# Performance work log

Hardware: AMD Instinct MI355X
Metric: run time of the kernel (lower is better)

The kernel has to match this reference:

```python
import jax, jax.numpy as jnp
import numpy as np

N = 100000
D = 128
R = 4
E = 1600000
LN_EPS = 1e-3  # keras LayerNormalization default epsilon


def setup_inputs() -> dict:
    key = jax.random.key(0)
    ks = jax.random.split(key, 12)
    return {
        "node_embeddings": jax.random.normal(ks[0], (N, D), jnp.float32),
        "rel_embeddings": jax.random.normal(ks[1], (R, D), jnp.float32),
        "adj_rows": jax.random.randint(ks[2], (R, E), 0, N, jnp.int32),
        "adj_cols": jax.random.randint(ks[3], (R, E), 0, N, jnp.int32),
        "adj_vals": jax.random.uniform(ks[4], (R, E), jnp.float32),
        "W_fuse": jax.random.normal(ks[5], (2 * D, D), jnp.float32) * 0.05,
        "b_fuse": jnp.zeros((D,), jnp.float32),
        "W_rel": jax.random.normal(ks[6], (R, D, D), jnp.float32) * 0.05,
        "b_rel": jnp.zeros((R, D), jnp.float32),
        "rel_weights": jnp.ones((R,), jnp.float32),
        "W_gate": jax.random.normal(ks[7], (D, D), jnp.float32) * 0.05,
        "b_gate": jnp.zeros((D,), jnp.float32),
        "ln_gamma": jnp.ones((D,), jnp.float32),
        "ln_beta": jnp.zeros((D,), jnp.float32),
    }


def reference(node_embeddings, rel_embeddings, adj_rows, adj_cols, adj_vals,
              W_fuse, b_fuse, W_rel, b_rel, rel_weights, W_gate, b_gate,
              ln_gamma, ln_beta):
    n = node_embeddings.shape[0]
    rel_outs = []
    for r in range(R):  # small fixed relation count, structurally distinct kernels
        # sparse-dense matmul: messages[i] = sum_j A_r[i,j] * X[j]
        gathered = adj_vals[r][:, None] * node_embeddings[adj_cols[r]]  # [E, D]
        messages = jax.ops.segment_sum(gathered, adj_rows[r], num_segments=n)  # [N, D]
        rel_vec = jnp.broadcast_to(rel_embeddings[r], messages.shape)
        cat = jnp.concatenate([messages, rel_vec], axis=-1)  # [N, 2D]
        fused = jax.nn.relu(cat @ W_fuse + b_fuse)  # [N, D]
        rel_outs.append(fused @ W_rel[r] + b_rel[r])  # relation-specific kernel
    stacked = jnp.stack(rel_outs, axis=0)  # [R, N, D]
    w = jax.nn.softmax(rel_weights)
    combined = jnp.einsum('r,rnd->nd', w, stacked)
    gate = jax.nn.sigmoid(node_embeddings @ W_gate + b_gate)
    x = node_embeddings + gate * combined
    mu = jnp.mean(x, axis=-1, keepdims=True)
    var = jnp.mean((x - mu) ** 2, axis=-1, keepdims=True)
    out = (x - mu) * jax.lax.rsqrt(var + LN_EPS) * ln_gamma + ln_beta
    return out  # dropout is identity at inference (training=None)
```

## Files before the change

### kernel.cpp

```cpp
#include <hip/hip_runtime.h>
#include <math.h>

#define N_NODES 100000
#define DIM 128
#define NREL 4
#define NEDGE 1600000
#define LN_EPS 1e-3f

#define NBUCK 196
#define BCAP 10240
#define P1_VPT 16
#define P1_EDGES 4096

typedef __attribute__((ext_vector_type(8))) short bf16x8;
typedef __attribute__((ext_vector_type(4))) float f32x4;

__device__ __forceinline__ float bf2f(unsigned short b) {
    return __uint_as_float(((unsigned int)b) << 16);
}
__device__ __forceinline__ unsigned short f2bf(float f) {
    unsigned int u = __float_as_uint(f);
    u += 0x7FFFu + ((u >> 16) & 1u);
    return (unsigned short)(u >> 16);
}

__global__ __launch_bounds__(512) void prep_kernel(
    const float* __restrict__ rel_emb, const float* __restrict__ W_fuse,
    const float* __restrict__ b_fuse, const float* __restrict__ rel_weights,
    float* __restrict__ bfr, float* __restrict__ wsm)
{
    int t = threadIdx.x;
    int r = t >> 7;
    int d = t & 127;
    float acc = b_fuse[d];
    for (int k = 0; k < DIM; ++k)
        acc += rel_emb[r * DIM + k] * W_fuse[(DIM + k) * DIM + d];
    bfr[r * DIM + d] = acc;
    if (t < NREL) {
        float m = rel_weights[0];
        for (int i = 1; i < NREL; ++i) m = fmaxf(m, rel_weights[i]);
        float s = 0.f;
        for (int i = 0; i < NREL; ++i) s += expf(rel_weights[i] - m);
        wsm[t] = expf(rel_weights[t] - m) / s;
    }
}

__global__ __launch_bounds__(256) void pack_kernel(
    const float* __restrict__ Wf, const float* __restrict__ Wr,
    const float* __restrict__ Wg,
    unsigned short* __restrict__ PH, unsigned short* __restrict__ PL)
{
    int mat = blockIdx.y;
    int idx = blockIdx.x * 256 + threadIdx.x;
    int j = idx & 7;
    int lane = (idx >> 3) & 63;
    int ntile = (idx >> 9) & 7;
    int kblk = idx >> 12;
    int k = kblk * 32 + (lane >> 4) * 8 + j;
    int n = ntile * 16 + (lane & 15);
    const float* src = (mat == 0) ? Wf :
                       (mat == 5) ? Wg : (Wr + (size_t)(mat - 1) * DIM * DIM);
    float w = src[k * DIM + n];
    unsigned short hi = f2bf(w);
    float lo = w - bf2f(hi);
    PH[mat * 16384 + idx] = hi;
    PL[mat * 16384 + idx] = f2bf(lo);
}

__global__ __launch_bounds__(256) void xb_kernel(
    const float* __restrict__ X, unsigned short* __restrict__ Xb)
{
    int idx = blockIdx.x * 256 + threadIdx.x;
    float4 f = ((const float4*)X)[idx];
    ushort4 o;
    o.x = f2bf(f.x); o.y = f2bf(f.y); o.z = f2bf(f.z); o.w = f2bf(f.w);
    ((ushort4*)Xb)[idx] = o;
}

__global__ __launch_bounds__(256) void y_kernel(
    const float* __restrict__ X,
    const unsigned short* __restrict__ PH,
    const unsigned short* __restrict__ PL,
    unsigned short* __restrict__ Yb)
{
    __shared__ unsigned short sXh[32 * 128];
    __shared__ unsigned short sXl[32 * 128];

    int t = threadIdx.x;
    int row0 = blockIdx.x * 32;
    int wv = t >> 6, l = t & 63, lq = l >> 4, lm = l & 15;

    const float4* Xs = (const float4*)(X + (size_t)row0 * DIM);
#pragma unroll
    for (int it = 0; it < 2; ++it) {
        int i = t + it * 256;
        float4 f0 = Xs[2 * i];
        float4 f1 = Xs[2 * i + 1];
        float e[8] = {f0.x, f0.y, f0.z, f0.w, f1.x, f1.y, f1.z, f1.w};
        unsigned short h[8], lo[8];
#pragma unroll
        for (int j = 0; j < 8; ++j) {
            h[j] = f2bf(e[j]);
            lo[j] = f2bf(e[j] - bf2f(h[j]));
        }
        uint4 hv, lv;
        hv.x = ((unsigned int)h[1] << 16) | h[0];
        hv.y = ((unsigned int)h[3] << 16) | h[2];
        hv.z = ((unsigned int)h[5] << 16) | h[4];
        hv.w = ((unsigned int)h[7] << 16) | h[6];
        lv.x = ((unsigned int)lo[1] << 16) | lo[0];
        lv.y = ((unsigned int)lo[3] << 16) | lo[2];
        lv.z = ((unsigned int)lo[5] << 16) | lo[4];
        lv.w = ((unsigned int)lo[7] << 16) | lo[6];
        int row = i >> 4, ck = i & 15;
        int off = row * 256 + ((ck * 16) ^ ((row & 7) << 4));
        *(uint4*)((char*)sXh + off) = hv;
        *(uint4*)((char*)sXl + off) = lv;
    }
    __syncthreads();

    f32x4 acc[2][2];
#pragma unroll
    for (int mt = 0; mt < 2; ++mt)
#pragma unroll
        for (int ni = 0; ni < 2; ++ni)
#pragma unroll
            for (int r = 0; r < 4; ++r) acc[mt][ni][r] = 0.f;

#pragma unroll
    for (int kb = 0; kb < 4; ++kb) {
        int c0 = kb * 64 + lq * 16;
        int r0 = lm, r1 = 16 + lm;
        int o0 = r0 * 256 + (c0 ^ ((r0 & 7) << 4));
        int o1 = r1 * 256 + (c0 ^ ((r1 & 7) << 4));
        bf16x8 ah0 = *(const bf16x8*)((char*)sXh + o0);
        bf16x8 ah1 = *(const bf16x8*)((char*)sXh + o1);
        bf16x8 al0 = *(const bf16x8*)((char*)sXl + o0);
        bf16x8 al1 = *(const bf16x8*)((char*)sXl + o1);
#pragma unroll
        for (int ni = 0; ni < 2; ++ni) {
            int nt_ = wv * 2 + ni;
            int fi = ((kb * 8 + nt_) * 64 + l) << 3;
            bf16x8 bh = *(const bf16x8*)(PH + fi);
            bf16x8 bl = *(const bf16x8*)(PL + fi);
            acc[0][ni] = __builtin_amdgcn_mfma_f32_16x16x32_bf16(ah0, bh, acc[0][ni], 0, 0, 0);
            acc[1][ni] = __builtin_amdgcn_mfma_f32_16x16x32_bf16(ah1, bh, acc[1][ni], 0, 0, 0);
            acc[0][ni] = __builtin_amdgcn_mfma_f32_16x16x32_bf16(ah0, bl, acc[0][ni], 0, 0, 0);
            acc[1][ni] = __builtin_amdgcn_mfma_f32_16x16x32_bf16(ah1, bl, acc[1][ni], 0, 0, 0);
            acc[0][ni] = __builtin_amdgcn_mfma_f32_16x16x32_bf16(al0, bh, acc[0][ni], 0, 0, 0);
            acc[1][ni] = __builtin_amdgcn_mfma_f32_16x16x32_bf16(al1, bh, acc[1][ni], 0, 0, 0);
        }
    }
    __syncthreads();
#pragma unroll
    for (int mt = 0; mt < 2; ++mt)
#pragma unroll
    for (int ni = 0; ni < 2; ++ni) {
        int colg = (wv * 2 + ni) * 16 + lm;
#pragma unroll
        for (int r = 0; r < 4; ++r) {
            int row = mt * 16 + lq * 4 + r;
            sXh[row * 128 + colg] = f2bf(acc[mt][ni][r]);
        }
    }
    __syncthreads();
    const uint4* s4 = (const uint4*)sXh;
#pragma unroll
    for (int it = 0; it < 2; ++it) {
        int i = t + it * 256;
        int row = i >> 4, ck = i & 15;
        int half = ck >> 3, c64 = ck & 7;
        uint4* dst = (uint4*)(Yb + (size_t)half * N_NODES * 64 +
                              (size_t)(row0 + row) * 64);
        dst[c64] = s4[i];
    }
}

__global__ __launch_bounds__(256) void binA_kernel(
    const int* __restrict__ arows, const int* __restrict__ acols,
    const float* __restrict__ avals,
    int* __restrict__ bcnt,
    unsigned long long* __restrict__ edges2)
{
    __shared__ int hist[256];
    __shared__ int hoff[256];
    __shared__ int gbase[NBUCK];
    __shared__ unsigned long long stage[P1_EDGES];
    __shared__ unsigned short sbid[P1_EDGES];

    int t = threadIdx.x;
    int rl = blockIdx.y;
    int e0 = blockIdx.x * P1_EDGES;

    hist[t] = 0;
    __syncthreads();

    int b[P1_VPT], rank[P1_VPT], rloc[P1_VPT];
    unsigned int pay[P1_VPT];
#pragma unroll
    for (int i = 0; i < P1_VPT; ++i) {
        int e = e0 + i * 256 + t;
        b[i] = -1;
        if (e < NEDGE) {
            size_t off = (size_t)rl * NEDGE + e;
            int row = arows[off];
            unsigned int vb = __float_as_uint(avals[off]);
            vb += 0x7FFFu + ((vb >> 16) & 1u);
            pay[i] = ((unsigned int)acols[off] << 15) | ((vb >> 16) & 0x7FFFu);
            b[i] = row >> 9;
            rloc[i] = row & 511;
            rank[i] = atomicAdd(&hist[b[i]], 1);
        }
    }
    __syncthreads();

    int v = hist[t];
    int run = v;
    hoff[t] = run;
    __syncthreads();
    for (int o = 1; o < 256; o <<= 1) {
        int other = (t >= o) ? hoff[t - o] : 0;
        __syncthreads();
        run += other;
        hoff[t] = run;
        __syncthreads();
    }
    hoff[t] = run - v;
    if (t < NBUCK) {
        int g = (v > 0) ? atomicAdd(&bcnt[rl * NBUCK + t], v) : 0;
        gbase[t] = (rl * NBUCK + t) * BCAP + g;
    }
    __syncthreads();

#pragma unroll
    for (int i = 0; i < P1_VPT; ++i) {
        if (b[i] >= 0) {
            int slot = hoff[b[i]] + rank[i];
            stage[slot] = ((unsigned long long)rloc[i] << 32) | pay[i];
            sbid[slot] = (unsigned short)b[i];
        }
    }
    __syncthreads();

    int total = hoff[NBUCK - 1] + hist[NBUCK - 1];
    for (int idx = t; idx < total; idx += 256) {
        int bb = sbid[idx];
        int gaddr = gbase[bb] + (idx - hoff[bb]);
        if (gaddr - (rl * NBUCK + bb) * BCAP < BCAP)
            edges2[gaddr] = stage[idx];
    }
}

__global__ __launch_bounds__(1024) void bscan_kernel(
    const int* __restrict__ bcnt, int* __restrict__ bstart)
{
    __shared__ int s[1024];
    int t = threadIdx.x;
    int v = (t < NREL * NBUCK) ? min(bcnt[t], BCAP) : 0;
    int run = v;
    s[t] = run;
    __syncthreads();
    for (int o = 1; o < 1024; o <<= 1) {
        int other = (t >= o) ? s[t - o] : 0;
        __syncthreads();
        run += other;
        s[t] = run;
        __syncthreads();
    }
    if (t < NREL * NBUCK) bstart[t] = run - v;
}

__global__ __launch_bounds__(256) void binB_kernel(
    const unsigned long long* __restrict__ edges2,
    const int* __restrict__ bcnt, const int* __restrict__ bstart,
    int* __restrict__ rowstart, unsigned int* __restrict__ edges)
{
    __shared__ int rcnt[512];
    __shared__ int rpos[512];
    __shared__ int sc[256];

    int t = threadIdx.x;
    int b = blockIdx.x, rl = blockIdx.y;
    int gb = rl * NBUCK + b;
    int cnt = min(bcnt[gb], BCAP);
    const unsigned long long* src = edges2 + (size_t)gb * BCAP;
    int row0 = b << 9;
    int nrows = min(512, N_NODES - row0);

    rcnt[t] = 0; rcnt[t + 256] = 0;
    __syncthreads();
    for (int e = t; e < cnt; e += 256)
        atomicAdd(&rcnt[(int)(src[e] >> 32)], 1);
    __syncthreads();

    int v0 = rcnt[2 * t], v1 = rcnt[2 * t + 1];
    int tsum = v0 + v1;
    int run = tsum;
    sc[t] = run;
    __syncthreads();
    for (int o = 1; o < 256; o <<= 1) {
        int other = (t >= o) ? sc[t - o] : 0;
        __syncthreads();
        run += other;
        sc[t] = run;
        __syncthreads();
    }
    int base = bstart[gb];
    int excl = base + run - tsum;
    rpos[2 * t] = excl;
    rpos[2 * t + 1] = excl + v0;
    __syncthreads();

    for (int i = t; i < nrows; i += 256)
        rowstart[rl * N_NODES + row0 + i] = rpos[i];
    __syncthreads();

    for (int e = t; e < cnt; e += 256) {
        unsigned long long s = src[e];
        int p = atomicAdd(&rpos[(int)(s >> 32)], 1);
        edges[p] = (unsigned int)s;
    }
}

#define FMA8(acc, v, q)                                    \
    acc[0] += v * __uint_as_float((q).x << 16);            \
    acc[1] += v * __uint_as_float((q).x & 0xFFFF0000u);    \
    acc[2] += v * __uint_as_float((q).y << 16);            \
    acc[3] += v * __uint_as_float((q).y & 0xFFFF0000u);    \
    acc[4] += v * __uint_as_float((q).z << 16);            \
    acc[5] += v * __uint_as_float((q).z & 0xFFFF0000u);    \
    acc[6] += v * __uint_as_float((q).w << 16);            \
    acc[7] += v * __uint_as_float((q).w & 0xFFFF0000u);

__global__ __launch_bounds__(256) void gather_kernel(
    const unsigned short* __restrict__ Yb,
    const int* __restrict__ rowstart,
    const unsigned int* __restrict__ edges,
    const float* __restrict__ bfr,
    unsigned short* __restrict__ msgs)
{
    int t = threadIdx.x;
    int grp = t >> 3, lane = t & 7;
    int row = blockIdx.x * 32 + grp;
    int rl = blockIdx.y & 3;
    int h  = blockIdx.y >> 2;
    int g = rl * N_NODES + row;
    int s = rowstart[g];
    int e = (g == NREL * N_NODES - 1) ? (NREL * NEDGE) : rowstart[g + 1];

    float a0[8], a1[8], a2[8], a3[8];
#pragma unroll
    for (int i = 0; i < 8; ++i) { a0[i] = 0.f; a1[i] = 0.f; a2[i] = 0.f; a3[i] = 0.f; }

    const uint4* Yb4 = (const uint4*)(Yb + (size_t)h * N_NODES * 64);
    int ee = s;
    int nrem = e - s;
    if (nrem >= 4) {
        unsigned int p0 = edges[ee], p1 = edges[ee + 1],
                     p2 = edges[ee + 2], p3 = edges[ee + 3];
        while (nrem >= 4) {
            uint4 q0 = Yb4[((size_t)(p0 >> 15) << 3) + lane];
            uint4 q1 = Yb4[((size_t)(p1 >> 15) << 3) + lane];
            uint4 q2 = Yb4[((size_t)(p2 >> 15) << 3) + lane];
            uint4 q3 = Yb4[((size_t)(p3 >> 15) << 3) + lane];
            float v0 = __uint_as_float((p0 & 0x7FFFu) << 16);
            float v1 = __uint_as_float((p1 & 0x7FFFu) << 16);
            float v2 = __uint_as_float((p2 & 0x7FFFu) << 16);
            float v3 = __uint_as_float((p3 & 0x7FFFu) << 16);
            nrem -= 4; ee += 4;
            if (nrem >= 4) {
                p0 = edges[ee + 0]; p1 = edges[ee + 1];
                p2 = edges[ee + 2]; p3 = edges[ee + 3];
            }
            FMA8(a0, v0, q0)
            FMA8(a1, v1, q1)
            FMA8(a2, v2, q2)
            FMA8(a3, v3, q3)
        }
    }
    while (nrem > 0) {
        unsigned int p = edges[ee];
        uint4 q = Yb4[((size_t)(p >> 15) << 3) + lane];
        float v = __uint_as_float((p & 0x7FFFu) << 16);
        FMA8(a0, v, q)
        ++ee; --nrem;
    }
#pragma unroll
    for (int i = 0; i < 8; ++i) a0[i] += a1[i] + a2[i] + a3[i];

    const float4* bb = (const float4*)(bfr + rl * DIM + h * 64 + lane * 8);
    float4 b0 = bb[0], b1 = bb[1];
    float f0 = fmaxf(a0[0] + b0.x, 0.f), f1 = fmaxf(a0[1] + b0.y, 0.f);
    float f2 = fmaxf(a0[2] + b0.z, 0.f), f3 = fmaxf(a0[3] + b0.w, 0.f);
    float f4 = fmaxf(a0[4] + b1.x, 0.f), f5 = fmaxf(a0[5] + b1.y, 0.f);
    float f6 = fmaxf(a0[6] + b1.z, 0.f), f7 = fmaxf(a0[7] + b1.w, 0.f);
    uint4 o;
    o.x = ((unsigned int)f2bf(f1) << 16) | f2bf(f0);
    o.y = ((unsigned int)f2bf(f3) << 16) | f2bf(f2);
    o.z = ((unsigned int)f2bf(f5) << 16) | f2bf(f4);
    o.w = ((unsigned int)f2bf(f7) << 16) | f2bf(f6);
    ((uint4*)(msgs + ((size_t)g << 7) + h * 64))[lane] = o;
}

__global__ __launch_bounds__(256) void gemm2_kernel(
    const unsigned short* __restrict__ msgs,
    const float* __restrict__ X,
    const unsigned short* __restrict__ PH,
    const unsigned short* __restrict__ PL,
    const float* __restrict__ br,
    const float* __restrict__ wsm,
    const float* __restrict__ bg,
    const float* __restrict__ gamma,
    const float* __restrict__ beta,
    float* __restrict__ out)
{
    __shared__ float sX[32 * 132];
    __shared__ float red[32][8], red2[32][8];
    __shared__ float smu[32], srs[32];
    unsigned short* sB = (unsigned short*)sX;

    int t = threadIdx.x;
    int row0 = blockIdx.x * 32;
    int wv = t >> 6, l = t & 63, lq = l >> 4, lm = l & 15;

    f32x4 comb[2][2];
#pragma unroll
    for (int mt = 0; mt < 2; ++mt)
#pragma unroll
        for (int ni = 0; ni < 2; ++ni)
#pragma unroll
            for (int r = 0; r < 4; ++r) comb[mt][ni][r] = 0.f;

    uint4 m0, m1;
    {
        const uint4* src = (const uint4*)msgs + ((size_t)row0 << 4);
        m0 = src[t]; m1 = src[t + 256];
    }
    float4 xa, xb_, xc, xd;

    for (int rl = 0; rl < NREL; ++rl) {
        __syncthreads();
        {
            int i0 = t, i1 = t + 256;
            int row = i0 >> 4, ck = i0 & 15;
            *(uint4*)((char*)sB + row * 256 + ((ck * 16) ^ ((row & 7) << 4))) = m0;
            row = i1 >> 4; ck = i1 & 15;
            *(uint4*)((char*)sB + row * 256 + ((ck * 16) ^ ((row & 7) << 4))) = m1;
        }
        if (rl < NREL - 1) {
            const uint4* src = (const uint4*)msgs +
                ((size_t)((rl + 1) * N_NODES + row0) << 4);
            m0 = src[t]; m1 = src[t + 256];
        } else {
            const float4* Xs = (const float4*)(X + (size_t)row0 * DIM);
            xa = Xs[2 * t];       xb_ = Xs[2 * t + 1];
            xc = Xs[2 * (t + 256)]; xd = Xs[2 * (t + 256) + 1];
        }
        __syncthreads();

        const unsigned short* ph2 = PH + (size_t)(1 + rl) * 16384;
        const unsigned short* pl2 = PL + (size_t)(1 + rl) * 16384;
        f32x4 acc[2][2];
#pragma unroll
        for (int mt = 0; mt < 2; ++mt)
#pragma unroll
            for (int ni = 0; ni < 2; ++ni)
#pragma unroll
                for (int r = 0; r < 4; ++r) acc[mt][ni][r] = 0.f;

#pragma unroll
        for (int kb = 0; kb < 4; ++kb) {
            int c0 = kb * 64 + lq * 16;
            int r0 = lm, r1 = 16 + lm;
            int o0 = r0 * 256 + (c0 ^ ((r0 & 7) << 4));
            int o1 = r1 * 256 + (c0 ^ ((r1 & 7) << 4));
            bf16x8 a0v = *(const bf16x8*)((char*)sB + o0);
            bf16x8 a1v = *(const bf16x8*)((char*)sB + o1);
#pragma unroll
            for (int ni = 0; ni < 2; ++ni) {
                int nt_ = wv * 2 + ni;
                int fi = ((kb * 8 + nt_) * 64 + l) << 3;
                bf16x8 bh = *(const bf16x8*)(ph2 + fi);
                bf16x8 bl = *(const bf16x8*)(pl2 + fi);
                acc[0][ni] = __builtin_amdgcn_mfma_f32_16x16x32_bf16(a0v, bh, acc[0][ni], 0, 0, 0);
                acc[1][ni] = __builtin_amdgcn_mfma_f32_16x16x32_bf16(a1v, bh, acc[1][ni], 0, 0, 0);
                acc[0][ni] = __builtin_amdgcn_mfma_f32_16x16x32_bf16(a0v, bl, acc[0][ni], 0, 0, 0);
                acc[1][ni] = __builtin_amdgcn_mfma_f32_16x16x32_bf16(a1v, bl, acc[1][ni], 0, 0, 0);
            }
        }
        {
            float wr_ = wsm[rl];
#pragma unroll
            for (int mt = 0; mt < 2; ++mt)
#pragma unroll
            for (int ni = 0; ni < 2; ++ni) {
                int colg = (wv * 2 + ni) * 16 + lm;
                float b = br[rl * DIM + colg];
#pragma unroll
                for (int r = 0; r < 4; ++r)
                    comb[mt][ni][r] += wr_ * (acc[mt][ni][r] + b);
            }
        }
    }

    __syncthreads();
    {
        float e0[8] = {xa.x, xa.y, xa.z, xa.w, xb_.x, xb_.y, xb_.z, xb_.w};
        uint4 hv;
        hv.x = ((unsigned int)f2bf(e0[1]) << 16) | f2bf(e0[0]);
        hv.y = ((unsigned int)f2bf(e0[3]) << 16) | f2bf(e0[2]);
        hv.z = ((unsigned int)f2bf(e0[5]) << 16) | f2bf(e0[4]);
        hv.w = ((unsigned int)f2bf(e0[7]) << 16) | f2bf(e0[6]);
        int i = t, row = i >> 4, ck = i & 15;
        *(uint4*)((char*)sB + row * 256 + ((ck * 16) ^ ((row & 7) << 4))) = hv;
        float e1[8] = {xc.x, xc.y, xc.z, xc.w, xd.x, xd.y, xd.z, xd.w};
        hv.x = ((unsigned int)f2bf(e1[1]) << 16) | f2bf(e1[0]);
        hv.y = ((unsigned int)f2bf(e1[3]) << 16) | f2bf(e1[2]);
        hv.z = ((unsigned int)f2bf(e1[5]) << 16) | f2bf(e1[4]);
        hv.w = ((unsigned int)f2bf(e1[7]) << 16) | f2bf(e1[6]);
        i = t + 256; row = i >> 4; ck = i & 15;
        *(uint4*)((char*)sB + row * 256 + ((ck * 16) ^ ((row & 7) << 4))) = hv;
    }
    __syncthreads();

    f32x4 accg[2][2];
#pragma unroll
    for (int mt = 0; mt < 2; ++mt)
#pragma unroll
        for (int ni = 0; ni < 2; ++ni)
#pragma unroll
            for (int r = 0; r < 4; ++r) accg[mt][ni][r] = 0.f;

    const unsigned short* phg = PH + (size_t)5 * 16384;
    const unsigned short* plg = PL + (size_t)5 * 16384;
#pragma unroll
    for (int kb = 0; kb < 4; ++kb) {
        int c0 = kb * 64 + lq * 16;
        int r0 = lm, r1 = 16 + lm;
        bf16x8 a0v = *(const bf16x8*)((char*)sB + r0 * 256 + (c0 ^ ((r0 & 7) << 4)));
        bf16x8 a1v = *(const bf16x8*)((char*)sB + r1 * 256 + (c0 ^ ((r1 & 7) << 4)));
#pragma unroll
        for (int ni = 0; ni < 2; ++ni) {
            int nt_ = wv * 2 + ni;
            int fi = ((kb * 8 + nt_) * 64 + l) << 3;
            bf16x8 bh = *(const bf16x8*)(phg + fi);
            bf16x8 bl = *(const bf16x8*)(plg + fi);
            accg[0][ni] = __builtin_amdgcn_mfma_f32_16x16x32_bf16(a0v, bh, accg[0][ni], 0, 0, 0);
            accg[1][ni] = __builtin_amdgcn_mfma_f32_16x16x32_bf16(a1v, bh, accg[1][ni], 0, 0, 0);
            accg[0][ni] = __builtin_amdgcn_mfma_f32_16x16x32_bf16(a0v, bl, accg[0][ni], 0, 0, 0);
            accg[1][ni] = __builtin_amdgcn_mfma_f32_16x16x32_bf16(a1v, bl, accg[1][ni], 0, 0, 0);
        }
    }
    __syncthreads();

    {
        int i = t, row = i >> 4, c = (i & 15) << 3;
        *(float4*)&sX[row * 132 + c] = xa;
        *(float4*)&sX[row * 132 + c + 4] = xb_;
        i = t + 256; row = i >> 4; c = (i & 15) << 3;
        *(float4*)&sX[row * 132 + c] = xc;
        *(float4*)&sX[row * 132 + c + 4] = xd;
    }
    __syncthreads();

#pragma unroll
    for (int mt = 0; mt < 2; ++mt)
#pragma unroll
    for (int ni = 0; ni < 2; ++ni) {
        int colg = (wv * 2 + ni) * 16 + lm;
        float bgv = bg[colg];
#pragma unroll
        for (int r = 0; r < 4; ++r) {
            int row = mt * 16 + lq * 4 + r;
            float g = 1.f / (1.f + expf(-(accg[mt][ni][r] + bgv)));
            sX[row * 132 + colg] += g * comb[mt][ni][r];
        }
    }
    __syncthreads();

    {
        int row = t >> 3, seg = t & 7;
        float s = 0.f, s2 = 0.f;
#pragma unroll
        for (int i = 0; i < 16; ++i) {
            float v = sX[row * 132 + seg * 16 + i];
            s += v; s2 += v * v;
        }
        red[row][seg] = s;
        red2[row][seg] = s2;
    }
    __syncthreads();
    if ((t & 7) == 0) {
        int row = t >> 3;
        float ts = 0.f, ts2 = 0.f;
#pragma unroll
        for (int i = 0; i < 8; ++i) { ts += red[row][i]; ts2 += red2[row][i]; }
        float mu = ts / DIM;
        float var = ts2 / DIM - mu * mu;
        smu[row] = mu;
        srs[row] = rsqrtf(var + LN_EPS);
    }
    __syncthreads();
    {
        float gm0 = gamma[l], gm1 = gamma[l + 64];
        float bt0 = beta[l],  bt1 = beta[l + 64];
#pragma unroll
        for (int rr = 0; rr < 8; ++rr) {
            int row = wv * 8 + rr;
            size_t gi = (size_t)(row0 + row) * DIM + l;
            out[gi]      = (sX[row * 132 + l]      - smu[row]) * srs[row] * gm0 + bt0;
            out[gi + 64] = (sX[row * 132 + l + 64] - smu[row]) * srs[row] * gm1 + bt1;
        }
    }
}

__global__ __launch_bounds__(256) void hist_kernel(
    const int* __restrict__ arows, int* __restrict__ counts)
{
    int e = blockIdx.x * 256 + threadIdx.x;
    int rl = blockIdx.y;
    if (e < NEDGE) {
        int row = arows[(size_t)rl * NEDGE + e];
        atomicAdd(&counts[rl * N_NODES + row], 1);
    }
}

__global__ __launch_bounds__(256) void scan1_kernel(
    int* __restrict__ counts, int* __restrict__ chunksums, int M)
{
    __shared__ int s[256];
    int chunk = blockIdx.x, t = threadIdx.x;
    int base = chunk * 1024 + t * 4;
    int v0 = (base + 0 < M) ? counts[base + 0] : 0;
    int v1 = (base + 1 < M) ? counts[base + 1] : 0;
    int v2 = (base + 2 < M) ? counts[base + 2] : 0;
    int v3 = (base + 3 < M) ? counts[base + 3] : 0;
    int p1 = v0, p2 = v0 + v1, p3 = v0 + v1 + v2, tsum = p3 + v3;
    int run = tsum;
    s[t] = run;
    __syncthreads();
    for (int off = 1; off < 256; off <<= 1) {
        int other = (t >= off) ? s[t - off] : 0;
        __syncthreads();
        run += other;
        s[t] = run;
        __syncthreads();
    }
    int excl = run - tsum;
    if (t == 255) chunksums[chunk] = run;
    if (base + 0 < M) counts[base + 0] = excl;
    if (base + 1 < M) counts[base + 1] = excl + p1;
    if (base + 2 < M) counts[base + 2] = excl + p2;
    if (base + 3 < M) counts[base + 3] = excl + p3;
}

__global__ __launch_bounds__(512) void scan2_kernel(
    int* __restrict__ chunksums, int nchunks)
{
    __shared__ int s[512];
    int t = threadIdx.x;
    int v = (t < nchunks) ? chunksums[t] : 0;
    int run = v;
    s[t] = run;
    __syncthreads();
    for (int off = 1; off < 512; off <<= 1) {
        int other = (t >= off) ? s[t - off] : 0;
        __syncthreads();
        run += other;
        s[t] = run;
        __syncthreads();
    }
    if (t < nchunks) chunksums[t] = run - v;
}

__global__ __launch_bounds__(256) void reorder_kernel(
    const int* __restrict__ arows, const int* __restrict__ acols,
    const float* __restrict__ avals,
    int* __restrict__ counts, const int* __restrict__ chunks,
    unsigned int* __restrict__ edges)
{
    int e = blockIdx.x * 256 + threadIdx.x;
    int rl = blockIdx.y;
    if (e < NEDGE) {
        size_t off = (size_t)rl * NEDGE + e;
        int row = arows[off];
        int g = rl * N_NODES + row;
        int pos = atomicAdd(&counts[g], 1) + chunks[g >> 10];
        unsigned int vb = __float_as_uint(avals[off]);
        vb += 0x7FFFu + ((vb >> 16) & 1u);
        edges[pos] = ((unsigned int)acols[off] << 15) | ((vb >> 16) & 0x7FFFu);
    }
}

__global__ __launch_bounds__(256) void mega_kernel(
    const unsigned short* __restrict__ Xb,
    const float* __restrict__ X,
    const int* __restrict__ counts,
    const int* __restrict__ chunks,
    const unsigned int* __restrict__ edges,
    const float* __restrict__ W1,
    const float* __restrict__ bfr,
    const float* __restrict__ Wr,
    const float* __restrict__ br,
    const float* __restrict__ wsm,
    const float* __restrict__ Wg,
    const float* __restrict__ bg,
    const float* __restrict__ gamma,
    const float* __restrict__ beta,
    float* __restrict__ out)
{
    __shared__ float sIn[32][DIM];
    __shared__ float red[32][8], red2[32][8];
    __shared__ float smu[32], srs[32];

    int t = threadIdx.x;
    int row0 = blockIdx.x * 32;
    int w = t >> 6;
    int l = t & 63;
    int grp = t >> 5, lane = t & 31;

    float comb_acc[8][2];
#pragma unroll
    for (int rr = 0; rr < 8; ++rr) { comb_acc[rr][0] = 0.f; comb_acc[rr][1] = 0.f; }

    for (int rl = 0; rl < NREL; ++rl) {
        __syncthreads();
#pragma unroll
        for (int i = 0; i < 4; ++i) {
            int ln = grp * 4 + i;
            int g = rl * N_NODES + row0 + ln;
            int s = (g == 0) ? 0 : counts[g - 1] + chunks[(g - 1) >> 10];
            int e = counts[g] + chunks[g >> 10];
            float4 a0 = make_float4(0.f, 0.f, 0.f, 0.f);
            int ee = s;
            for (; ee < e; ++ee) {
                unsigned int p0 = edges[ee];
                const ushort4* x0 = (const ushort4*)(Xb + ((size_t)(p0 >> 15) << 7));
                ushort4 q0 = x0[lane];
                float v0 = __uint_as_float((p0 & 0x7FFFu) << 16);
                a0.x += v0 * bf2f(q0.x); a0.y += v0 * bf2f(q0.y);
                a0.z += v0 * bf2f(q0.z); a0.w += v0 * bf2f(q0.w);
            }
            ((float4*)&sIn[ln][0])[lane] = a0;
        }
        __syncthreads();

        float acc1[8][2];
#pragma unroll
        for (int rr = 0; rr < 8; ++rr) { acc1[rr][0] = 0.f; acc1[rr][1] = 0.f; }
        for (int k4 = 0; k4 < DIM / 4; ++k4) {
            float wa[4], wb4[4];
#pragma unroll
            for (int j = 0; j < 4; ++j) {
                wa[j]  = W1[(k4 * 4 + j) * DIM + l];
                wb4[j] = W1[(k4 * 4 + j) * DIM + l + 64];
            }
#pragma unroll
            for (int rr = 0; rr < 8; ++rr) {
                float4 m = *(const float4*)&sIn[w * 8 + rr][k4 * 4];
                acc1[rr][0] += m.x * wa[0]  + m.y * wa[1]  + m.z * wa[2]  + m.w * wa[3];
                acc1[rr][1] += m.x * wb4[0] + m.y * wb4[1] + m.z * wb4[2] + m.w * wb4[3];
            }
        }
        __syncthreads();
        {
            float b0 = bfr[rl * DIM + l], b1 = bfr[rl * DIM + l + 64];
#pragma unroll
            for (int rr = 0; rr < 8; ++rr) {
                sIn[w * 8 + rr][l]      = fmaxf(acc1[rr][0] + b0, 0.f);
                sIn[w * 8 + rr][l + 64] = fmaxf(acc1[rr][1] + b1, 0.f);
            }
        }
        __syncthreads();

        const float* W2 = Wr + (size_t)rl * DIM * DIM;
        float acc2[8][2];
#pragma unroll
        for (int rr = 0; rr < 8; ++rr) { acc2[rr][0] = 0.f; acc2[rr][1] = 0.f; }
        for (int k4 = 0; k4 < DIM / 4; ++k4) {
            float wa[4], wb4[4];
#pragma unroll
            for (int j = 0; j < 4; ++j) {
                wa[j]  = W2[(k4 * 4 + j) * DIM + l];
                wb4[j] = W2[(k4 * 4 + j) * DIM + l + 64];
            }
#pragma unroll
            for (int rr = 0; rr < 8; ++rr) {
                float4 m = *(const float4*)&sIn[w * 8 + rr][k4 * 4];
                acc2[rr][0] += m.x * wa[0]  + m.y * wa[1]  + m.z * wa[2]  + m.w * wa[3];
                acc2[rr][1] += m.x * wb4[0] + m.y * wb4[1] + m.z * wb4[2] + m.w * wb4[3];
            }
        }
        {
            float wr_ = wsm[rl];
            float bb0 = br[rl * DIM + l], bb1 = br[rl * DIM + l + 64];
#pragma unroll
            for (int rr = 0; rr < 8; ++rr) {
                comb_acc[rr][0] += wr_ * (acc2[rr][0] + bb0);
                comb_acc[rr][1] += wr_ * (acc2[rr][1] + bb1);
            }
        }
    }

    __syncthreads();
    {
        const float4* src = (const float4*)(X + (size_t)row0 * DIM);
        float4* dst = (float4*)&sIn[0][0];
        for (int i = t; i < 32 * DIM / 4; i += 256) dst[i] = src[i];
    }
    __syncthreads();

    float accg[8][2];
#pragma unroll
    for (int rr = 0; rr < 8; ++rr) { accg[rr][0] = 0.f; accg[rr][1] = 0.f; }
    for (int k4 = 0; k4 < DIM / 4; ++k4) {
        float wa[4], wb4[4];
#pragma unroll
        for (int j = 0; j < 4; ++j) {
            wa[j]  = Wg[(k4 * 4 + j) * DIM + l];
            wb4[j] = Wg[(k4 * 4 + j) * DIM + l + 64];
        }
#pragma unroll
        for (int rr = 0; rr < 8; ++rr) {
            float4 m = *(const float4*)&sIn[w * 8 + rr][k4 * 4];
            accg[rr][0] += m.x * wa[0]  + m.y * wa[1]  + m.z * wa[2]  + m.w * wa[3];
            accg[rr][1] += m.x * wb4[0] + m.y * wb4[1] + m.z * wb4[2] + m.w * wb4[3];
        }
    }
    float xv[8][2];
    {
        float bg0 = bg[l], bg1 = bg[l + 64];
#pragma unroll
        for (int rr = 0; rr < 8; ++rr) {
            int row = w * 8 + rr;
            float g0 = 1.f / (1.f + expf(-(accg[rr][0] + bg0)));
            float g1 = 1.f / (1.f + expf(-(accg[rr][1] + bg1)));
            xv[rr][0] = sIn[row][l]      + g0 * comb_acc[rr][0];
            xv[rr][1] = sIn[row][l + 64] + g1 * comb_acc[rr][1];
        }
    }
    __syncthreads();
#pragma unroll
    for (int rr = 0; rr < 8; ++rr) {
        sIn[w * 8 + rr][l]      = xv[rr][0];
        sIn[w * 8 + rr][l + 64] = xv[rr][1];
    }
    __syncthreads();

    {
        int row = t >> 3, seg = t & 7;
        float s = 0.f, s2 = 0.f;
#pragma unroll
        for (int i = 0; i < 16; ++i) {
            float v = sIn[row][seg * 16 + i];
            s += v; s2 += v * v;
        }
        red[row][seg] = s;
        red2[row][seg] = s2;
    }
    __syncthreads();
    if ((t & 7) == 0) {
        int row = t >> 3;
        float ts = 0.f, ts2 = 0.f;
#pragma unroll
        for (int i = 0; i < 8; ++i) { ts += red[row][i]; ts2 += red2[row][i]; }
        float mu = ts / DIM;
        float var = ts2 / DIM - mu * mu;
        smu[row] = mu;
        srs[row] = rsqrtf(var + LN_EPS);
    }
    __syncthreads();
    {
        float gm0 = gamma[l], gm1 = gamma[l + 64];
        float bt0 = beta[l],  bt1 = beta[l + 64];
#pragma unroll
        for (int rr = 0; rr < 8; ++rr) {
            int row = w * 8 + rr;
            size_t gi = (size_t)(row0 + row) * DIM + l;
            out[gi]      = (sIn[row][l]      - smu[row]) * srs[row] * gm0 + bt0;
            out[gi + 64] = (sIn[row][l + 64] - smu[row]) * srs[row] * gm1 + bt1;
        }
    }
}

extern "C" void kernel_launch(void* const* d_in, const int* in_sizes, int n_in,
                              void* d_out, int out_size, void* d_ws, size_t ws_size,
                              hipStream_t stream) {
    const float* X     = (const float*)d_in[0];
    const float* rel   = (const float*)d_in[1];
    const int*   arows = (const int*)d_in[2];
    const int*   acols = (const int*)d_in[3];
    const float* avals = (const float*)d_in[4];
    const float* Wf    = (const float*)d_in[5];
    const float* bf    = (const float*)d_in[6];
    const float* Wr    = (const float*)d_in[7];
    const float* br    = (const float*)d_in[8];
    const float* rw    = (const float*)d_in[9];
    const float* Wg    = (const float*)d_in[10];
    const float* bg    = (const float*)d_in[11];
    const float* gamma = (const float*)d_in[12];
    const float* beta  = (const float*)d_in[13];
    float* out = (float*)d_out;

    const size_t XB_B = (size_t)N_NODES * DIM * 2;
    const size_t ED_B = (size_t)NREL * NEDGE * 4;
    const size_t CT_B = (size_t)NREL * N_NODES * 4;
    char* p = (char*)d_ws;
    unsigned short* Yb     = (unsigned short*)p;  p += XB_B;
    unsigned int*   edges  = (unsigned int*)p;    p += ED_B;
    int*            counts = (int*)p;             p += CT_B;
    int*            chunks = (int*)p;             p += 512 * 4;
    float*          bfr    = (float*)p;           p += NREL * DIM * 4;
    float*          wsm    = (float*)p;           p += 64 * 4;
    int*            bcnt   = (int*)p;             p += NREL * NBUCK * 4;
    int*            bstart = (int*)p;             p += (NREL * NBUCK + 1) * 4;
    unsigned short* PH     = (unsigned short*)p;  p += 6 * 16384 * 2;
    unsigned short* PL     = (unsigned short*)p;  p += 6 * 16384 * 2;
    size_t off = (size_t)(p - (char*)d_ws);
    off = (off + 255) & ~(size_t)255;
    unsigned short* msgs = (unsigned short*)((char*)d_ws + off);
    unsigned long long* edges2 = (unsigned long long*)msgs;
    const size_t need = off + (size_t)NREL * N_NODES * DIM * 2;
    const bool split = (ws_size >= need);

    prep_kernel<<<1, 512, 0, stream>>>(rel, Wf, bf, rw, bfr, wsm);
    pack_kernel<<<dim3(64, 6), 256, 0, stream>>>(Wf, Wr, Wg, PH, PL);

    if (split) {
        y_kernel<<<N_NODES / 32, 256, 0, stream>>>(X, PH, PL, Yb);
        hipMemsetAsync(bcnt, 0, (size_t)NREL * NBUCK * sizeof(int), stream);
        const int AB = (NEDGE + P1_EDGES - 1) / P1_EDGES;
        binA_kernel<<<dim3(AB, NREL), 256, 0, stream>>>(
            arows, acols, avals, bcnt, edges2);
        bscan_kernel<<<1, 1024, 0, stream>>>(bcnt, bstart);
        binB_kernel<<<dim3(NBUCK, NREL), 256, 0, stream>>>(
            edges2, bcnt, bstart, counts, edges);
        gather_kernel<<<dim3(N_NODES / 32, NREL * 2), 256, 0, stream>>>(
            Yb, counts, edges, bfr, msgs);
        gemm2_kernel<<<N_NODES / 32, 256, 0, stream>>>(
            msgs, X, PH, PL, br, wsm, bg, gamma, beta, out);
    } else {
        xb_kernel<<<N_NODES * DIM / 4 / 256, 256, 0, stream>>>(X, Yb);
        const int EB = (NEDGE + 255) / 256;
        const int M = NREL * N_NODES;
        const int nch = (M + 1023) / 1024;
        hipMemsetAsync(counts, 0, (size_t)M * sizeof(int), stream);
        hist_kernel<<<dim3(EB, NREL), 256, 0, stream>>>(arows, counts);
        scan1_kernel<<<nch, 256, 0, stream>>>(counts, chunks, M);
        scan2_kernel<<<1, 512, 0, stream>>>(chunks, nch);
        reorder_kernel<<<dim3(EB, NREL), 256, 0, stream>>>(
            arows, acols, avals, counts, chunks, edges);
        mega_kernel<<<N_NODES / 32, 256, 0, stream>>>(
            Yb, X, counts, chunks, edges, Wf, bfr, Wr, br, wsm,
            Wg, bg, gamma, beta, out);
    }
}
```

Before: 598.1 us.

## Split gather feature table into quarters and pad bucket counters

The projected node table Yb is now stored as four 32-column planes instead of two 64-column planes. The gather kernel is relaunched with four column-quarter slices per relation, and each row is handled by 4 lanes instead of 8, so every gathered row touches a smaller 64-byte span and the working set per plane shrinks for cache locality. Separately, the per-bucket atomic counters are padded to a 16-int stride so that atomics from different buckets do not share a cache line. The cost is that edge lists are read twice as many times, once per quarter, and there are more blocks in total.

```diff
diff --git a/kernel.cpp b/kernel.cpp
--- a/kernel.cpp
+++ b/kernel.cpp
@@ -11,6 +11,7 @@
 #define BCAP 10240
 #define P1_VPT 16
 #define P1_EDGES 4096
+#define BCNT_STRIDE 16
 
 typedef __attribute__((ext_vector_type(8))) short bf16x8;
 typedef __attribute__((ext_vector_type(4))) float f32x4;
@@ -169,10 +170,10 @@
     for (int it = 0; it < 2; ++it) {
         int i = t + it * 256;
         int row = i >> 4, ck = i & 15;
-        int half = ck >> 3, c64 = ck & 7;
-        uint4* dst = (uint4*)(Yb + (size_t)half * N_NODES * 64 +
-                              (size_t)(row0 + row) * 64);
-        dst[c64] = s4[i];
+        int q = ck >> 2, c32 = ck & 3;
+        uint4* dst = (uint4*)(Yb + (size_t)q * N_NODES * 32 +
+                              (size_t)(row0 + row) * 32);
+        dst[c32] = s4[i];
     }
 }
 
@@ -227,7 +228,7 @@
     }
     hoff[t] = run - v;
     if (t < NBUCK) {
-        int g = (v > 0) ? atomicAdd(&bcnt[rl * NBUCK + t], v) : 0;
+        int g = (v > 0) ? atomicAdd(&bcnt[(rl * NBUCK + t) * BCNT_STRIDE], v) : 0;
         gbase[t] = (rl * NBUCK + t) * BCAP + g;
     }
     __syncthreads();
@@ -256,7 +257,7 @@
 {
     __shared__ int s[1024];
     int t = threadIdx.x;
-    int v = (t < NREL * NBUCK) ? min(bcnt[t], BCAP) : 0;
+    int v = (t < NREL * NBUCK) ? min(bcnt[t * BCNT_STRIDE], BCAP) : 0;
     int run = v;
     s[t] = run;
     __syncthreads();
@@ -282,7 +283,7 @@
     int t = threadIdx.x;
     int b = blockIdx.x, rl = blockIdx.y;
     int gb = rl * NBUCK + b;
-    int cnt = min(bcnt[gb], BCAP);
+    int cnt = min(bcnt[gb * BCNT_STRIDE], BCAP);
     const unsigned long long* src = edges2 + (size_t)gb * BCAP;
     int row0 = b << 9;
     int nrows = min(512, N_NODES - row0);
@@ -340,10 +341,11 @@
     unsigned short* __restrict__ msgs)
 {
     int t = threadIdx.x;
-    int grp = t >> 3, lane = t & 7;
-    int row = blockIdx.x * 32 + grp;
+    int grp = t >> 2, lane = t & 3;
+    int row = blockIdx.x * 64 + grp;
+    if (row >= N_NODES) return;
     int rl = blockIdx.y & 3;
-    int h  = blockIdx.y >> 2;
+    int q  = blockIdx.y >> 2;
     int g = rl * N_NODES + row;
     int s = rowstart[g];
     int e = (g == NREL * N_NODES - 1) ? (NREL * NEDGE) : rowstart[g + 1];
@@ -352,17 +354,17 @@
 #pragma unroll
     for (int i = 0; i < 8; ++i) { a0[i] = 0.f; a1[i] = 0.f; a2[i] = 0.f; a3[i] = 0.f; }
 
-    const uint4* Yb4 = (const uint4*)(Yb + (size_t)h * N_NODES * 64);
+    const uint4* Yb4 = (const uint4*)(Yb + (size_t)q * N_NODES * 32);
     int ee = s;
     int nrem = e - s;
     if (nrem >= 4) {
         unsigned int p0 = edges[ee], p1 = edges[ee + 1],
                      p2 = edges[ee + 2], p3 = edges[ee + 3];
         while (nrem >= 4) {
-            uint4 q0 = Yb4[((size_t)(p0 >> 15) << 3) + lane];
-            uint4 q1 = Yb4[((size_t)(p1 >> 15) << 3) + lane];
-            uint4 q2 = Yb4[((size_t)(p2 >> 15) << 3) + lane];
-            uint4 q3 = Yb4[((size_t)(p3 >> 15) << 3) + lane];
+            uint4 q0 = Yb4[((size_t)(p0 >> 15) << 2) + lane];
+            uint4 q1 = Yb4[((size_t)(p1 >> 15) << 2) + lane];
+            uint4 q2 = Yb4[((size_t)(p2 >> 15) << 2) + lane];
+            uint4 q3 = Yb4[((size_t)(p3 >> 15) << 2) + lane];
             float v0 = __uint_as_float((p0 & 0x7FFFu) << 16);
             float v1 = __uint_as_float((p1 & 0x7FFFu) << 16);
             float v2 = __uint_as_float((p2 & 0x7FFFu) << 16);
@@ -380,15 +382,15 @@
     }
     while (nrem > 0) {
         unsigned int p = edges[ee];
-        uint4 q = Yb4[((size_t)(p >> 15) << 3) + lane];
+        uint4 qq = Yb4[((size_t)(p >> 15) << 2) + lane];
         float v = __uint_as_float((p & 0x7FFFu) << 16);
-        FMA8(a0, v, q)
+        FMA8(a0, v, qq)
         ++ee; --nrem;
     }
 #pragma unroll
     for (int i = 0; i < 8; ++i) a0[i] += a1[i] + a2[i] + a3[i];
 
-    const float4* bb = (const float4*)(bfr + rl * DIM + h * 64 + lane * 8);
+    const float4* bb = (const float4*)(bfr + rl * DIM + q * 32 + lane * 8);
     float4 b0 = bb[0], b1 = bb[1];
     float f0 = fmaxf(a0[0] + b0.x, 0.f), f1 = fmaxf(a0[1] + b0.y, 0.f);
     float f2 = fmaxf(a0[2] + b0.z, 0.f), f3 = fmaxf(a0[3] + b0.w, 0.f);
@@ -399,7 +401,7 @@
     o.y = ((unsigned int)f2bf(f3) << 16) | f2bf(f2);
     o.z = ((unsigned int)f2bf(f5) << 16) | f2bf(f4);
     o.w = ((unsigned int)f2bf(f7) << 16) | f2bf(f6);
-    ((uint4*)(msgs + ((size_t)g << 7) + h * 64))[lane] = o;
+    ((uint4*)(msgs + ((size_t)g << 7) + q * 32))[lane] = o;
 }
 
 __global__ __launch_bounds__(256) void gemm2_kernel(
@@ -912,7 +914,7 @@
     int*            chunks = (int*)p;             p += 512 * 4;
     float*          bfr    = (float*)p;           p += NREL * DIM * 4;
     float*          wsm    = (float*)p;           p += 64 * 4;
-    int*            bcnt   = (int*)p;             p += NREL * NBUCK * 4;
+    int*            bcnt   = (int*)p;             p += NREL * NBUCK * BCNT_STRIDE * 4;
     int*            bstart = (int*)p;             p += (NREL * NBUCK + 1) * 4;
     unsigned short* PH     = (unsigned short*)p;  p += 6 * 16384 * 2;
     unsigned short* PL     = (unsigned short*)p;  p += 6 * 16384 * 2;
@@ -928,14 +930,15 @@
 
     if (split) {
         y_kernel<<<N_NODES / 32, 256, 0, stream>>>(X, PH, PL, Yb);
-        hipMemsetAsync(bcnt, 0, (size_t)NREL * NBUCK * sizeof(int), stream);
+        hipMemsetAsync(bcnt, 0,
+                       (size_t)NREL * NBUCK * BCNT_STRIDE * sizeof(int), stream);
         const int AB = (NEDGE + P1_EDGES - 1) / P1_EDGES;
         binA_kernel<<<dim3(AB, NREL), 256, 0, stream>>>(
             arows, acols, avals, bcnt, edges2);
         bscan_kernel<<<1, 1024, 0, stream>>>(bcnt, bstart);
         binB_kernel<<<dim3(NBUCK, NREL), 256, 0, stream>>>(
             edges2, bcnt, bstart, counts, edges);
-        gather_kernel<<<dim3(N_NODES / 32, NREL * 2), 256, 0, stream>>>(
+        gather_kernel<<<dim3((N_NODES + 63) / 64, NREL * 4), 256, 0, stream>>>(
             Yb, counts, edges, bfr, msgs);
         gemm2_kernel<<<N_NODES / 32, 256, 0, stream>>>(
             msgs, X, PH, PL, br, wsm, bg, gamma, beta, out);
```

Measured after the change: 668.8 us. +11.8%, slower.
